# Kernel tuning notes

Hardware: AMD Instinct MI355X
Metric: run time of the kernel (lower is better)

The kernel has to match this reference:

```python
import jax, jax.numpy as jnp
import numpy as np

N_NODES = 10000
N_EDGES = 640000
D = 128


def _sage_conv(x, src, dst, W_l, b, W_r):
    # PyG SAGEConv (mean aggr): out = lin_l(mean_{j in N(i)} x_j) + lin_r(x_i)
    msgs = x[src]                                        # [E, D_in] gather
    agg = jax.ops.segment_sum(msgs, dst, num_segments=N_NODES)  # [N, D_in]
    deg = jax.ops.segment_sum(jnp.ones((src.shape[0],), x.dtype), dst,
                              num_segments=N_NODES)
    agg = agg / jnp.maximum(deg, 1.0)[:, None]           # mean; isolated nodes -> 0
    return agg @ W_l + b + x @ W_r


def setup_inputs() -> dict:
    key = jax.random.key(0)
    ks = jax.random.split(key, 8)
    s = 1.0 / np.sqrt(D)
    return {
        "x": jax.random.normal(ks[0], (N_NODES, D), dtype=jnp.float32),
        "edge_index": jax.random.randint(ks[1], (2, N_EDGES), 0, N_NODES, dtype=jnp.int64),
        "W_l0": jax.random.normal(ks[2], (D, D), dtype=jnp.float32) * s,
        "b0": jnp.zeros((D,), dtype=jnp.float32),
        "W_r0": jax.random.normal(ks[3], (D, D), dtype=jnp.float32) * s,
        "W_l1": jax.random.normal(ks[4], (D, D), dtype=jnp.float32) * s,
        "b1": jnp.zeros((D,), dtype=jnp.float32),
        "W_r1": jax.random.normal(ks[5], (D, D), dtype=jnp.float32) * s,
    }


def reference(x, edge_index, W_l0, b0, W_r0, W_l1, b1, W_r1):
    # Dropout(p=0.3) is identity in eval mode (reference runs inference math).
    src, dst = edge_index[0], edge_index[1]
    h = jax.nn.elu(_sage_conv(x, src, dst, W_l0, b0, W_r0))
    h = jax.nn.elu(_sage_conv(h, src, dst, W_l1, b1, W_r1))
    return h
```

## Files before the change

kernel.cpp:

```cpp
#include <hip/hip_runtime.h>

#define N_NODES 10000
#define N_EDGES 640000
#define D 128
#define MAXDEG 128
#define NBUCK 157
#define BCAP 6144
#define EPT 5
#define ZROW 10000

typedef unsigned int uint;
typedef unsigned short u16;
typedef short bf16x8 __attribute__((ext_vector_type(8)));
typedef float f32x4 __attribute__((ext_vector_type(4)));

__device__ __forceinline__ u16 f2bf(float f) {
    uint u = __float_as_uint(f);
    return (u16)((u + 0x7fffu + ((u >> 16) & 1u)) >> 16);
}
__device__ __forceinline__ float bflo(uint v) { return __uint_as_float(v << 16); }
__device__ __forceinline__ float bfhi(uint v) { return __uint_as_float(v & 0xffff0000u); }

__device__ __forceinline__ int edge_at(const void* ei, int is32, int idx) {
    if (is32) return ((const int*)ei)[idx];
    return (int)((const long long*)ei)[idx];
}

__global__ __launch_bounds__(256)
void binp1_kernel(const void* __restrict__ ei, int* __restrict__ gcount,
                  uint* __restrict__ gbucket) {
    __shared__ int hist[NBUCK];
    __shared__ int base[NBUCK];
    __shared__ int s_is32;
    const int t = threadIdx.x;
    if (t < NBUCK) hist[t] = 0;
    if (t == 0) s_is32 = 0;
    __syncthreads();
    const int e0 = blockIdx.x * (256 * EPT);
    if (((const int*)ei)[2 * (e0 + t) + 1] != 0) s_is32 = 1;
    __syncthreads();
    const int is32 = s_is32;
    uint pk[EPT];
    int  rk[EPT];
#pragma unroll
    for (int i = 0; i < EPT; ++i) {
        int e  = e0 + i * 256 + t;
        int s  = edge_at(ei, is32, e);
        int dn = edge_at(ei, is32, N_EDGES + e);
        pk[i] = ((uint)dn << 16) | (uint)s;
        rk[i] = atomicAdd(&hist[dn >> 6], 1);
    }
    __syncthreads();
    if (t < NBUCK) base[t] = atomicAdd(&gcount[t], hist[t]);
    __syncthreads();
#pragma unroll
    for (int i = 0; i < EPT; ++i) {
        int bkt = (int)(pk[i] >> 22);
        int pos = base[bkt] + rk[i];
        if (pos < BCAP) gbucket[(size_t)bkt * BCAP + pos] = pk[i];
    }
}

__global__ __launch_bounds__(256)
void prep_kernel(const int* __restrict__ gcount, const uint* __restrict__ gbucket,
                 u16* __restrict__ adj, int* __restrict__ deg_g,
                 const float* __restrict__ x, uint* __restrict__ xb2,
                 const float* __restrict__ Wl0, const float* __restrict__ Wr0,
                 const float* __restrict__ Wl1, const float* __restrict__ Wr1,
                 u16* __restrict__ WT0, u16* __restrict__ WT1) {
    const int b = blockIdx.x;
    const int t = threadIdx.x;
    __shared__ __align__(16) u16 tile[64][MAXDEG];
    __shared__ int cur[64];
    if (b < NBUCK) {
        uint* tw = (uint*)&tile[0][0];
#pragma unroll
        for (int q = 0; q < 16; ++q) tw[t + q * 256] = ((uint)ZROW << 16) | ZROW;
        if (t < 64) cur[t] = 0;
        __syncthreads();
        const int total = min(gcount[b], BCAP);
        for (int e = t; e < total; e += 256) {
            uint pk = gbucket[(size_t)b * BCAP + e];
            int ln = (int)((pk >> 16) & 63u);
            int r = atomicAdd(&cur[ln], 1);
            if (r < MAXDEG) tile[ln][r] = (u16)(pk & 0xffffu);
        }
        __syncthreads();
        const int node0 = b * 64;
        if (t < 64 && node0 + t < N_NODES) deg_g[node0 + t] = cur[t];
        const uint4* ts = (const uint4*)&tile[0][0];
#pragma unroll
        for (int q = 0; q < 4; ++q) {
            int i = t + q * 256;
            int node = node0 + (i >> 4);
            if (node < N_NODES) ((uint4*)(adj + (size_t)node * MAXDEG))[i & 15] = ts[i];
        }
    } else if (b < NBUCK + 625) {
        int idx = (b - NBUCK) * 256 + t;
        const float4* p = (const float4*)x + (size_t)idx * 2;
        float4 a = p[0], bb = p[1];
        uint4 r;
        r.x = (uint)f2bf(a.x) | ((uint)f2bf(a.y) << 16);
        r.y = (uint)f2bf(a.z) | ((uint)f2bf(a.w) << 16);
        r.z = (uint)f2bf(bb.x) | ((uint)f2bf(bb.y) << 16);
        r.w = (uint)f2bf(bb.z) | ((uint)f2bf(bb.w) << 16);
        ((uint4*)xb2)[idx] = r;
    } else if (b < NBUCK + 625 + 256) {
        int b2 = b - (NBUCK + 625);
        int layer = b2 >> 7, d = b2 & 127, k = t;
        const float* Wl = layer ? Wl1 : Wl0;
        const float* Wr = layer ? Wr1 : Wr0;
        u16* WT = layer ? WT1 : WT0;
        float v = (k < 128) ? Wl[k * D + d] : Wr[(k - 128) * D + d];
        WT[(size_t)d * 256 + k] = f2bf(v);
    } else {
        if (t < 16) ((uint4*)(xb2 + (size_t)ZROW * 64))[t] = make_uint4(0, 0, 0, 0);
    }
}

__global__ __launch_bounds__(256)
void gather_kernel(const uint* __restrict__ xb2, const u16* __restrict__ adj,
                   const int* __restrict__ deg_g, uint* __restrict__ aggb2) {
    const int node = blockIdx.x * 4 + (threadIdx.x >> 6);
    const int l = threadIdx.x & 63;
    const int g = l >> 4;
    const int c = l & 15;
    const int half = g >> 1;
    const int sh = (g & 1) << 4;
    const int dg = deg_g[node];
    const int cnt = min(dg, MAXDEG);
    const uint4* __restrict__ rowq = (const uint4*)(adj + (size_t)node * MAXDEG);
    float acc[8];
#pragma unroll
    for (int i = 0; i < 8; ++i) acc[i] = 0.f;
    const int nch = (cnt + 15) >> 4;
#pragma unroll 2
    for (int ch = 0; ch < nch; ++ch) {
        uint4 wa = rowq[2 * ch];
        uint4 wb = rowq[2 * ch + 1];
        uint a0 = half ? wa.y : wa.x;
        uint a1 = half ? wa.w : wa.z;
        uint b0 = half ? wb.y : wb.x;
        uint b1 = half ? wb.w : wb.z;
        uint id0 = (a0 >> sh) & 0xffffu;
        uint id1 = (a1 >> sh) & 0xffffu;
        uint id2 = (b0 >> sh) & 0xffffu;
        uint id3 = (b1 >> sh) & 0xffffu;
        uint4 v0 = ((const uint4*)(xb2 + (size_t)id0 * 64))[c];
        uint4 v1 = ((const uint4*)(xb2 + (size_t)id1 * 64))[c];
        uint4 v2 = ((const uint4*)(xb2 + (size_t)id2 * 64))[c];
        uint4 v3 = ((const uint4*)(xb2 + (size_t)id3 * 64))[c];
        acc[0] += bflo(v0.x) + bflo(v1.x) + bflo(v2.x) + bflo(v3.x);
        acc[1] += bfhi(v0.x) + bfhi(v1.x) + bfhi(v2.x) + bfhi(v3.x);
        acc[2] += bflo(v0.y) + bflo(v1.y) + bflo(v2.y) + bflo(v3.y);
        acc[3] += bfhi(v0.y) + bfhi(v1.y) + bfhi(v2.y) + bfhi(v3.y);
        acc[4] += bflo(v0.z) + bflo(v1.z) + bflo(v2.z) + bflo(v3.z);
        acc[5] += bfhi(v0.z) + bfhi(v1.z) + bfhi(v2.z) + bfhi(v3.z);
        acc[6] += bflo(v0.w) + bflo(v1.w) + bflo(v2.w) + bflo(v3.w);
        acc[7] += bfhi(v0.w) + bfhi(v1.w) + bfhi(v2.w) + bfhi(v3.w);
    }
#pragma unroll
    for (int i = 0; i < 8; ++i) {
        float r = acc[i];
        r += __shfl_xor(r, 16, 64);
        r += __shfl_xor(r, 32, 64);
        acc[i] = r;
    }
    if (g == 0) {
        float inv = 1.0f / fmaxf((float)dg, 1.0f);
        uint4 o;
        o.x = (uint)f2bf(acc[0] * inv) | ((uint)f2bf(acc[1] * inv) << 16);
        o.y = (uint)f2bf(acc[2] * inv) | ((uint)f2bf(acc[3] * inv) << 16);
        o.z = (uint)f2bf(acc[4] * inv) | ((uint)f2bf(acc[5] * inv) << 16);
        o.w = (uint)f2bf(acc[6] * inv) | ((uint)f2bf(acc[7] * inv) << 16);
        ((uint4*)(aggb2 + (size_t)node * 64))[c] = o;
    }
}

__global__ __launch_bounds__(256)
void mfma_gemm_kernel(const uint* __restrict__ aggb2, const uint* __restrict__ xb2,
                      const u16* __restrict__ WT, const float* __restrict__ bias,
                      float* __restrict__ outf ,
                      u16* __restrict__ outb ) {
    __shared__ __align__(16) u16 A_lds[16 * 256];
    const int t = threadIdx.x;
    const int nb = blockIdx.x * 16;
    {
        const int row = t >> 4, c = t & 15;
        const int node = nb + row;
        uint4 va = ((const uint4*)(aggb2 + (size_t)node * 64))[c];
        uint4 vx = ((const uint4*)(xb2  + (size_t)node * 64))[c];
        char* base = (char*)A_lds + row * 512;
        const int swz = (row & 7) << 4;
        *(uint4*)(base + ((c * 16) ^ swz))       = va;
        *(uint4*)(base + ((256 + c * 16) ^ swz)) = vx;
    }
    __syncthreads();

    const int w = t >> 6, l = t & 63;
    const int lr = l & 15, g = l >> 4;
    f32x4 acc0 = {0.f, 0.f, 0.f, 0.f}, acc1 = {0.f, 0.f, 0.f, 0.f};
    const char* abase = (const char*)A_lds + lr * 512;
    const int aswz = (lr & 7) << 4;
    const u16* wt0 = WT + (size_t)(w * 32 + lr) * 256;
    const u16* wt1 = WT + (size_t)(w * 32 + 16 + lr) * 256;
#pragma unroll
    for (int kk = 0; kk < 8; ++kk) {
        bf16x8 af  = *(const bf16x8*)(abase + ((kk * 64 + g * 16) ^ aswz));
        bf16x8 bf0 = *(const bf16x8*)(wt0 + kk * 32 + g * 8);
        bf16x8 bf1 = *(const bf16x8*)(wt1 + kk * 32 + g * 8);
        acc0 = __builtin_amdgcn_mfma_f32_16x16x32_bf16(af, bf0, acc0, 0, 0, 0);
        acc1 = __builtin_amdgcn_mfma_f32_16x16x32_bf16(af, bf1, acc1, 0, 0, 0);
    }

    const int col0 = w * 32 + lr, col1 = col0 + 16;
    const float b0v = bias[col0], b1v = bias[col1];
#pragma unroll
    for (int j = 0; j < 4; ++j) {
        const int node = nb + g * 4 + j;
        float v0 = acc0[j] + b0v; v0 = v0 > 0.f ? v0 : expm1f(v0);
        float v1 = acc1[j] + b1v; v1 = v1 > 0.f ? v1 : expm1f(v1);
        if (outf) {
            outf[(size_t)node * D + col0] = v0;
            outf[(size_t)node * D + col1] = v1;
        }
        if (outb) {
            outb[(size_t)node * D + col0] = f2bf(v0);
            outb[(size_t)node * D + col1] = f2bf(v1);
        }
    }
    if (outb && blockIdx.x == 0 && t < 16)
        ((uint4*)(outb + (size_t)ZROW * D))[t] = make_uint4(0, 0, 0, 0);
}

extern "C" void kernel_launch(void* const* d_in, const int* in_sizes, int n_in,
                              void* d_out, int out_size, void* d_ws, size_t ws_size,
                              hipStream_t stream) {
    const float* x   = (const float*)d_in[0];
    const void*  ei  = d_in[1];
    const float* Wl0 = (const float*)d_in[2];
    const float* b0  = (const float*)d_in[3];
    const float* Wr0 = (const float*)d_in[4];
    const float* Wl1 = (const float*)d_in[5];
    const float* b1  = (const float*)d_in[6];
    const float* Wr1 = (const float*)d_in[7];
    float* out = (float*)d_out;

    char* ws = (char*)d_ws;
    int*  gcount  = (int*)(ws + 1024);
    int*  deg     = (int*)(ws + 4096);
    u16*  adj     = (u16*)(ws + 65536);
    uint* gbucket = (uint*)(ws + 3145728);
    uint* yb2     = (uint*)(ws + 3145728);
    uint* aggb2   = (uint*)(ws + 5705984);
    uint* xb2     = (uint*)(ws + 8266240);
    u16*  WT0     = (u16*)(ws + 10826752);
    u16*  WT1     = (u16*)(ws + 10892288);

    hipMemsetAsync(ws, 0, 4096, stream);

    binp1_kernel<<<500, 256, 0, stream>>>(ei, gcount, gbucket);
    prep_kernel<<<NBUCK + 625 + 256 + 1, 256, 0, stream>>>(
        gcount, gbucket, adj, deg, x, xb2, Wl0, Wr0, Wl1, Wr1, WT0, WT1);

    gather_kernel<<<2500, 256, 0, stream>>>(xb2, adj, deg, aggb2);
    mfma_gemm_kernel<<<625, 256, 0, stream>>>(aggb2, xb2, WT0, b0, (float*)0, (u16*)yb2);

    gather_kernel<<<2500, 256, 0, stream>>>(yb2, adj, deg, aggb2);
    mfma_gemm_kernel<<<625, 256, 0, stream>>>(aggb2, yb2, WT1, b1, out, (u16*)0);
}
```

Baseline: 79.84 us.

## Fuse neighbor gather and MFMA linear layer into one kernel per layer

Merges the per-node mean-aggregation gather and the bf16 MFMA GEMM into a single kernel, so the aggregated row goes into LDS instead of a global aggb2 buffer. That removes two launches and the global write and read of the intermediate. Each block now handles only 4 nodes, so the 16-row MFMA tiles are three-quarters zero padding. The 128x256 weight matrix is also reloaded by every one of 2500 blocks rather than 625, which adds MFMA and weight-load cost. Workspace offsets are rearranged so the x and y buffers no longer overlap.

```diff
diff --git a/kernel.cpp b/kernel.cpp
--- a/kernel.cpp
+++ b/kernel.cpp
@@ -119,14 +119,19 @@
 }
 
 __global__ __launch_bounds__(256)
-void gather_kernel(const uint* __restrict__ xb2, const u16* __restrict__ adj,
-                   const int* __restrict__ deg_g, uint* __restrict__ aggb2) {
-    const int node = blockIdx.x * 4 + (threadIdx.x >> 6);
-    const int l = threadIdx.x & 63;
-    const int g = l >> 4;
-    const int c = l & 15;
-    const int half = g >> 1;
-    const int sh = (g & 1) << 4;
+void fused_layer_kernel(const uint* __restrict__ src2, const u16* __restrict__ adj,
+                        const int* __restrict__ deg_g, const u16* __restrict__ WT,
+                        const float* __restrict__ bias,
+                        float* __restrict__ outf ,
+                        u16* __restrict__ outb ) {
+    __shared__ __align__(16) u16 A_lds[4][256];
+    const int t = threadIdx.x;
+    const int w = t >> 6, l = t & 63;
+    const int nb = blockIdx.x * 4;
+    const int node = nb + w;
+
+    const int g = l >> 4, c = l & 15;
+    const int half = g >> 1, sh = (g & 1) << 4;
     const int dg = deg_g[node];
     const int cnt = min(dg, MAXDEG);
     const uint4* __restrict__ rowq = (const uint4*)(adj + (size_t)node * MAXDEG);
@@ -146,10 +151,10 @@
         uint id1 = (a1 >> sh) & 0xffffu;
         uint id2 = (b0 >> sh) & 0xffffu;
         uint id3 = (b1 >> sh) & 0xffffu;
-        uint4 v0 = ((const uint4*)(xb2 + (size_t)id0 * 64))[c];
-        uint4 v1 = ((const uint4*)(xb2 + (size_t)id1 * 64))[c];
-        uint4 v2 = ((const uint4*)(xb2 + (size_t)id2 * 64))[c];
-        uint4 v3 = ((const uint4*)(xb2 + (size_t)id3 * 64))[c];
+        uint4 v0 = ((const uint4*)(src2 + (size_t)id0 * 64))[c];
+        uint4 v1 = ((const uint4*)(src2 + (size_t)id1 * 64))[c];
+        uint4 v2 = ((const uint4*)(src2 + (size_t)id2 * 64))[c];
+        uint4 v3 = ((const uint4*)(src2 + (size_t)id3 * 64))[c];
         acc[0] += bflo(v0.x) + bflo(v1.x) + bflo(v2.x) + bflo(v3.x);
         acc[1] += bfhi(v0.x) + bfhi(v1.x) + bfhi(v2.x) + bfhi(v3.x);
         acc[2] += bflo(v0.y) + bflo(v1.y) + bflo(v2.y) + bflo(v3.y);
@@ -166,6 +171,8 @@
         r += __shfl_xor(r, 32, 64);
         acc[i] = r;
     }
+    char* arow = (char*)&A_lds[w][0];
+    const int swz = w << 4;
     if (g == 0) {
         float inv = 1.0f / fmaxf((float)dg, 1.0f);
         uint4 o;
@@ -173,60 +180,45 @@
         o.y = (uint)f2bf(acc[2] * inv) | ((uint)f2bf(acc[3] * inv) << 16);
         o.z = (uint)f2bf(acc[4] * inv) | ((uint)f2bf(acc[5] * inv) << 16);
         o.w = (uint)f2bf(acc[6] * inv) | ((uint)f2bf(acc[7] * inv) << 16);
-        ((uint4*)(aggb2 + (size_t)node * 64))[c] = o;
-    }
-}
-
-__global__ __launch_bounds__(256)
-void mfma_gemm_kernel(const uint* __restrict__ aggb2, const uint* __restrict__ xb2,
-                      const u16* __restrict__ WT, const float* __restrict__ bias,
-                      float* __restrict__ outf ,
-                      u16* __restrict__ outb ) {
-    __shared__ __align__(16) u16 A_lds[16 * 256];
-    const int t = threadIdx.x;
-    const int nb = blockIdx.x * 16;
-    {
-        const int row = t >> 4, c = t & 15;
-        const int node = nb + row;
-        uint4 va = ((const uint4*)(aggb2 + (size_t)node * 64))[c];
-        uint4 vx = ((const uint4*)(xb2  + (size_t)node * 64))[c];
-        char* base = (char*)A_lds + row * 512;
-        const int swz = (row & 7) << 4;
-        *(uint4*)(base + ((c * 16) ^ swz))       = va;
-        *(uint4*)(base + ((256 + c * 16) ^ swz)) = vx;
-    }
-    __syncthreads();
-
-    const int w = t >> 6, l = t & 63;
-    const int lr = l & 15, g = l >> 4;
+        *(uint4*)(arow + ((c * 16) ^ swz)) = o;
+    }
+    if (l < 16) {
+        uint4 vx = ((const uint4*)(src2 + (size_t)node * 64))[l];
+        *(uint4*)(arow + ((256 + l * 16) ^ swz)) = vx;
+    }
+    __syncthreads();
+
+    const int lr = l & 15, q = l >> 4;
     f32x4 acc0 = {0.f, 0.f, 0.f, 0.f}, acc1 = {0.f, 0.f, 0.f, 0.f};
-    const char* abase = (const char*)A_lds + lr * 512;
-    const int aswz = (lr & 7) << 4;
     const u16* wt0 = WT + (size_t)(w * 32 + lr) * 256;
     const u16* wt1 = WT + (size_t)(w * 32 + 16 + lr) * 256;
+    const char* abase = (const char*)&A_lds[lr & 3][0];
+    const int aswz = (lr & 3) << 4;
 #pragma unroll
     for (int kk = 0; kk < 8; ++kk) {
-        bf16x8 af  = *(const bf16x8*)(abase + ((kk * 64 + g * 16) ^ aswz));
-        bf16x8 bf0 = *(const bf16x8*)(wt0 + kk * 32 + g * 8);
-        bf16x8 bf1 = *(const bf16x8*)(wt1 + kk * 32 + g * 8);
+        bf16x8 af = {0, 0, 0, 0, 0, 0, 0, 0};
+        if (lr < 4) af = *(const bf16x8*)(abase + ((kk * 64 + q * 16) ^ aswz));
+        bf16x8 bf0 = *(const bf16x8*)(wt0 + kk * 32 + q * 8);
+        bf16x8 bf1 = *(const bf16x8*)(wt1 + kk * 32 + q * 8);
         acc0 = __builtin_amdgcn_mfma_f32_16x16x32_bf16(af, bf0, acc0, 0, 0, 0);
         acc1 = __builtin_amdgcn_mfma_f32_16x16x32_bf16(af, bf1, acc1, 0, 0, 0);
     }
-
-    const int col0 = w * 32 + lr, col1 = col0 + 16;
-    const float b0v = bias[col0], b1v = bias[col1];
-#pragma unroll
-    for (int j = 0; j < 4; ++j) {
-        const int node = nb + g * 4 + j;
-        float v0 = acc0[j] + b0v; v0 = v0 > 0.f ? v0 : expm1f(v0);
-        float v1 = acc1[j] + b1v; v1 = v1 > 0.f ? v1 : expm1f(v1);
-        if (outf) {
-            outf[(size_t)node * D + col0] = v0;
-            outf[(size_t)node * D + col1] = v1;
-        }
-        if (outb) {
-            outb[(size_t)node * D + col0] = f2bf(v0);
-            outb[(size_t)node * D + col1] = f2bf(v1);
+    if (q == 0) {
+        const int col0 = w * 32 + lr, col1 = col0 + 16;
+        const float b0v = bias[col0], b1v = bias[col1];
+#pragma unroll
+        for (int j = 0; j < 4; ++j) {
+            const int nd = nb + j;
+            float v0 = acc0[j] + b0v; v0 = v0 > 0.f ? v0 : expm1f(v0);
+            float v1 = acc1[j] + b1v; v1 = v1 > 0.f ? v1 : expm1f(v1);
+            if (outf) {
+                outf[(size_t)nd * D + col0] = v0;
+                outf[(size_t)nd * D + col1] = v1;
+            }
+            if (outb) {
+                outb[(size_t)nd * D + col0] = f2bf(v0);
+                outb[(size_t)nd * D + col1] = f2bf(v1);
+            }
         }
     }
     if (outb && blockIdx.x == 0 && t < 16)
@@ -251,11 +243,10 @@
     int*  deg     = (int*)(ws + 4096);
     u16*  adj     = (u16*)(ws + 65536);
     uint* gbucket = (uint*)(ws + 3145728);
-    uint* yb2     = (uint*)(ws + 3145728);
-    uint* aggb2   = (uint*)(ws + 5705984);
-    uint* xb2     = (uint*)(ws + 8266240);
-    u16*  WT0     = (u16*)(ws + 10826752);
-    u16*  WT1     = (u16*)(ws + 10892288);
+    uint* xb2     = (uint*)(ws + 7340032);
+    uint* yb2     = (uint*)(ws + 10485760);
+    u16*  WT0     = (u16*)(ws + 13631488);
+    u16*  WT1     = (u16*)(ws + 13697024);
 
     hipMemsetAsync(ws, 0, 4096, stream);
 
@@ -263,9 +254,8 @@
     prep_kernel<<<NBUCK + 625 + 256 + 1, 256, 0, stream>>>(
         gcount, gbucket, adj, deg, x, xb2, Wl0, Wr0, Wl1, Wr1, WT0, WT1);
 
-    gather_kernel<<<2500, 256, 0, stream>>>(xb2, adj, deg, aggb2);
-    mfma_gemm_kernel<<<625, 256, 0, stream>>>(aggb2, xb2, WT0, b0, (float*)0, (u16*)yb2);
-
-    gather_kernel<<<2500, 256, 0, stream>>>(yb2, adj, deg, aggb2);
-    mfma_gemm_kernel<<<625, 256, 0, stream>>>(aggb2, yb2, WT1, b1, out, (u16*)0);
-}
+    fused_layer_kernel<<<2500, 256, 0, stream>>>(xb2, adj, deg, WT0, b0,
+                                                 (float*)0, (u16*)yb2);
+    fused_layer_kernel<<<2500, 256, 0, stream>>>(yb2, adj, deg, WT1, b1,
+                                                 out, (u16*)0);
+}
```

Result: slower. 95.71 us (+19.9%).

## Replace global-atomic edge binning with per-chunk fixed segments and merge prep kernels

Applied to the files above, without the earlier changes.

Edge binning now writes each chunk's edges into a fixed per-(bucket, chunk) segment of 64 slots with a per-chunk count table, instead of reserving space through global atomics on bucket counters. That removes the hipMemsetAsync and folds the binning, x-to-bf16 conversion and weight transpose into a single launch, followed by a separate sort kernel that scans 500 chunk segments per bucket. The sort kernel now does many small, partly idle segment reads (each wave handles one chunk at a time), and edges beyond 64 per chunk-bucket pair would be dropped silently. For random edges that overflow is unlikely, but it is not guaranteed.

```diff
diff --git a/kernel.cpp b/kernel.cpp
--- a/kernel.cpp
+++ b/kernel.cpp
@@ -5,8 +5,9 @@
 #define D 128
 #define MAXDEG 128
 #define NBUCK 157
-#define BCAP 6144
-#define EPT 5
+#define NCHUNK 500
+#define CH_E 1280
+#define CSEG 64
 #define ZROW 10000
 
 typedef unsigned int uint;
@@ -27,76 +28,43 @@
 }
 
 __global__ __launch_bounds__(256)
-void binp1_kernel(const void* __restrict__ ei, int* __restrict__ gcount,
-                  uint* __restrict__ gbucket) {
-    __shared__ int hist[NBUCK];
-    __shared__ int base[NBUCK];
-    __shared__ int s_is32;
-    const int t = threadIdx.x;
-    if (t < NBUCK) hist[t] = 0;
-    if (t == 0) s_is32 = 0;
-    __syncthreads();
-    const int e0 = blockIdx.x * (256 * EPT);
-    if (((const int*)ei)[2 * (e0 + t) + 1] != 0) s_is32 = 1;
-    __syncthreads();
-    const int is32 = s_is32;
-    uint pk[EPT];
-    int  rk[EPT];
-#pragma unroll
-    for (int i = 0; i < EPT; ++i) {
-        int e  = e0 + i * 256 + t;
-        int s  = edge_at(ei, is32, e);
-        int dn = edge_at(ei, is32, N_EDGES + e);
-        pk[i] = ((uint)dn << 16) | (uint)s;
-        rk[i] = atomicAdd(&hist[dn >> 6], 1);
-    }
-    __syncthreads();
-    if (t < NBUCK) base[t] = atomicAdd(&gcount[t], hist[t]);
-    __syncthreads();
-#pragma unroll
-    for (int i = 0; i < EPT; ++i) {
-        int bkt = (int)(pk[i] >> 22);
-        int pos = base[bkt] + rk[i];
-        if (pos < BCAP) gbucket[(size_t)bkt * BCAP + pos] = pk[i];
-    }
-}
-
-__global__ __launch_bounds__(256)
-void prep_kernel(const int* __restrict__ gcount, const uint* __restrict__ gbucket,
-                 u16* __restrict__ adj, int* __restrict__ deg_g,
-                 const float* __restrict__ x, uint* __restrict__ xb2,
-                 const float* __restrict__ Wl0, const float* __restrict__ Wr0,
-                 const float* __restrict__ Wl1, const float* __restrict__ Wr1,
-                 u16* __restrict__ WT0, u16* __restrict__ WT1) {
+void binbig_kernel(const void* __restrict__ ei, u16* __restrict__ cnt,
+                   uint* __restrict__ gbucket2, const float* __restrict__ x,
+                   uint* __restrict__ xb2, uint* __restrict__ yb2,
+                   const float* __restrict__ Wl0, const float* __restrict__ Wr0,
+                   const float* __restrict__ Wl1, const float* __restrict__ Wr1,
+                   u16* __restrict__ WT0, u16* __restrict__ WT1) {
     const int b = blockIdx.x;
     const int t = threadIdx.x;
-    __shared__ __align__(16) u16 tile[64][MAXDEG];
-    __shared__ int cur[64];
-    if (b < NBUCK) {
-        uint* tw = (uint*)&tile[0][0];
-#pragma unroll
-        for (int q = 0; q < 16; ++q) tw[t + q * 256] = ((uint)ZROW << 16) | ZROW;
-        if (t < 64) cur[t] = 0;
+    if (b < NCHUNK) {
+        __shared__ int hist[NBUCK];
+        __shared__ int s_is32;
+        if (t < NBUCK) hist[t] = 0;
+        if (t == 0) s_is32 = 0;
         __syncthreads();
-        const int total = min(gcount[b], BCAP);
-        for (int e = t; e < total; e += 256) {
-            uint pk = gbucket[(size_t)b * BCAP + e];
-            int ln = (int)((pk >> 16) & 63u);
-            int r = atomicAdd(&cur[ln], 1);
-            if (r < MAXDEG) tile[ln][r] = (u16)(pk & 0xffffu);
-        }
+        if (((const int*)ei)[2 * t + 1] != 0) s_is32 = 1;
         __syncthreads();
-        const int node0 = b * 64;
-        if (t < 64 && node0 + t < N_NODES) deg_g[node0 + t] = cur[t];
-        const uint4* ts = (const uint4*)&tile[0][0];
-#pragma unroll
-        for (int q = 0; q < 4; ++q) {
-            int i = t + q * 256;
-            int node = node0 + (i >> 4);
-            if (node < N_NODES) ((uint4*)(adj + (size_t)node * MAXDEG))[i & 15] = ts[i];
-        }
-    } else if (b < NBUCK + 625) {
-        int idx = (b - NBUCK) * 256 + t;
+        const int is32 = s_is32;
+        const int e0 = b * CH_E;
+        uint pk[5]; int rk[5];
+#pragma unroll
+        for (int i = 0; i < 5; ++i) {
+            int e  = e0 + i * 256 + t;
+            int s  = edge_at(ei, is32, e);
+            int dn = edge_at(ei, is32, N_EDGES + e);
+            pk[i] = ((uint)dn << 16) | (uint)s;
+            rk[i] = atomicAdd(&hist[dn >> 6], 1);
+        }
+        __syncthreads();
+        if (t < NBUCK) cnt[(size_t)b * NBUCK + t] = (u16)min(hist[t], CSEG);
+#pragma unroll
+        for (int i = 0; i < 5; ++i) {
+            int bkt = (int)(pk[i] >> 22);
+            if (rk[i] < CSEG)
+                gbucket2[(size_t)bkt * (NCHUNK * CSEG) + b * CSEG + rk[i]] = pk[i];
+        }
+    } else if (b < NCHUNK + 625) {
+        int idx = (b - NCHUNK) * 256 + t;
         const float4* p = (const float4*)x + (size_t)idx * 2;
         float4 a = p[0], bb = p[1];
         uint4 r;
@@ -105,8 +73,8 @@
         r.z = (uint)f2bf(bb.x) | ((uint)f2bf(bb.y) << 16);
         r.w = (uint)f2bf(bb.z) | ((uint)f2bf(bb.w) << 16);
         ((uint4*)xb2)[idx] = r;
-    } else if (b < NBUCK + 625 + 256) {
-        int b2 = b - (NBUCK + 625);
+    } else if (b < NCHUNK + 625 + 256) {
+        int b2 = b - (NCHUNK + 625);
         int layer = b2 >> 7, d = b2 & 127, k = t;
         const float* Wl = layer ? Wl1 : Wl0;
         const float* Wr = layer ? Wr1 : Wr0;
@@ -114,7 +82,45 @@
         float v = (k < 128) ? Wl[k * D + d] : Wr[(k - 128) * D + d];
         WT[(size_t)d * 256 + k] = f2bf(v);
     } else {
-        if (t < 16) ((uint4*)(xb2 + (size_t)ZROW * 64))[t] = make_uint4(0, 0, 0, 0);
+        if (t < 16) {
+            ((uint4*)(xb2 + (size_t)ZROW * 64))[t] = make_uint4(0, 0, 0, 0);
+            ((uint4*)(yb2 + (size_t)ZROW * 64))[t] = make_uint4(0, 0, 0, 0);
+        }
+    }
+}
+
+__global__ __launch_bounds__(256)
+void sort_kernel(const u16* __restrict__ cnt, const uint* __restrict__ gbucket2,
+                 u16* __restrict__ adj, int* __restrict__ deg_g) {
+    __shared__ __align__(16) u16 tile[64][MAXDEG];
+    __shared__ int cur[64];
+    const int b = blockIdx.x;
+    const int t = threadIdx.x;
+    const int w = t >> 6, l = t & 63;
+    uint* tw = (uint*)&tile[0][0];
+#pragma unroll
+    for (int q = 0; q < 16; ++q) tw[t + q * 256] = ((uint)ZROW << 16) | ZROW;
+    if (t < 64) cur[t] = 0;
+    __syncthreads();
+    const uint* __restrict__ seg = gbucket2 + (size_t)b * (NCHUNK * CSEG);
+    for (int c = w; c < NCHUNK; c += 4) {
+        int n = cnt[(size_t)c * NBUCK + b];
+        if (l < n) {
+            uint pk = seg[c * CSEG + l];
+            int ln = (int)((pk >> 16) & 63u);
+            int r = atomicAdd(&cur[ln], 1);
+            if (r < MAXDEG) tile[ln][r] = (u16)(pk & 0xffffu);
+        }
+    }
+    __syncthreads();
+    const int node0 = b * 64;
+    if (t < 64 && node0 + t < N_NODES) deg_g[node0 + t] = cur[t];
+    const uint4* ts = (const uint4*)&tile[0][0];
+#pragma unroll
+    for (int q = 0; q < 4; ++q) {
+        int i = t + q * 256;
+        int node = node0 + (i >> 4);
+        if (node < N_NODES) ((uint4*)(adj + (size_t)node * MAXDEG))[i & 15] = ts[i];
     }
 }
 
@@ -128,12 +134,12 @@
     const int half = g >> 1;
     const int sh = (g & 1) << 4;
     const int dg = deg_g[node];
-    const int cnt = min(dg, MAXDEG);
+    const int cnt_ = min(dg, MAXDEG);
     const uint4* __restrict__ rowq = (const uint4*)(adj + (size_t)node * MAXDEG);
     float acc[8];
 #pragma unroll
     for (int i = 0; i < 8; ++i) acc[i] = 0.f;
-    const int nch = (cnt + 15) >> 4;
+    const int nch = (cnt_ + 15) >> 4;
 #pragma unroll 2
     for (int ch = 0; ch < nch; ++ch) {
         uint4 wa = rowq[2 * ch];
@@ -198,7 +204,7 @@
     __syncthreads();
 
     const int w = t >> 6, l = t & 63;
-    const int lr = l & 15, g = l >> 4;
+    const int lr = l & 15, q = l >> 4;
     f32x4 acc0 = {0.f, 0.f, 0.f, 0.f}, acc1 = {0.f, 0.f, 0.f, 0.f};
     const char* abase = (const char*)A_lds + lr * 512;
     const int aswz = (lr & 7) << 4;
@@ -206,9 +212,9 @@
     const u16* wt1 = WT + (size_t)(w * 32 + 16 + lr) * 256;
 #pragma unroll
     for (int kk = 0; kk < 8; ++kk) {
-        bf16x8 af  = *(const bf16x8*)(abase + ((kk * 64 + g * 16) ^ aswz));
-        bf16x8 bf0 = *(const bf16x8*)(wt0 + kk * 32 + g * 8);
-        bf16x8 bf1 = *(const bf16x8*)(wt1 + kk * 32 + g * 8);
+        bf16x8 af  = *(const bf16x8*)(abase + ((kk * 64 + q * 16) ^ aswz));
+        bf16x8 bf0 = *(const bf16x8*)(wt0 + kk * 32 + q * 8);
+        bf16x8 bf1 = *(const bf16x8*)(wt1 + kk * 32 + q * 8);
         acc0 = __builtin_amdgcn_mfma_f32_16x16x32_bf16(af, bf0, acc0, 0, 0, 0);
         acc1 = __builtin_amdgcn_mfma_f32_16x16x32_bf16(af, bf1, acc1, 0, 0, 0);
     }
@@ -217,7 +223,7 @@
     const float b0v = bias[col0], b1v = bias[col1];
 #pragma unroll
     for (int j = 0; j < 4; ++j) {
-        const int node = nb + g * 4 + j;
+        const int node = nb + q * 4 + j;
         float v0 = acc0[j] + b0v; v0 = v0 > 0.f ? v0 : expm1f(v0);
         float v1 = acc1[j] + b1v; v1 = v1 > 0.f ? v1 : expm1f(v1);
         if (outf) {
@@ -229,8 +235,6 @@
             outb[(size_t)node * D + col1] = f2bf(v1);
         }
     }
-    if (outb && blockIdx.x == 0 && t < 16)
-        ((uint4*)(outb + (size_t)ZROW * D))[t] = make_uint4(0, 0, 0, 0);
 }
 
 extern "C" void kernel_launch(void* const* d_in, const int* in_sizes, int n_in,
@@ -247,25 +251,24 @@
     float* out = (float*)d_out;
 
     char* ws = (char*)d_ws;
-    int*  gcount  = (int*)(ws + 1024);
-    int*  deg     = (int*)(ws + 4096);
-    u16*  adj     = (u16*)(ws + 65536);
-    uint* gbucket = (uint*)(ws + 3145728);
-    uint* yb2     = (uint*)(ws + 3145728);
-    uint* aggb2   = (uint*)(ws + 5705984);
-    uint* xb2     = (uint*)(ws + 8266240);
-    u16*  WT0     = (u16*)(ws + 10826752);
-    u16*  WT1     = (u16*)(ws + 10892288);
-
-    hipMemsetAsync(ws, 0, 4096, stream);
-
-    binp1_kernel<<<500, 256, 0, stream>>>(ei, gcount, gbucket);
-    prep_kernel<<<NBUCK + 625 + 256 + 1, 256, 0, stream>>>(
-        gcount, gbucket, adj, deg, x, xb2, Wl0, Wr0, Wl1, Wr1, WT0, WT1);
+    u16*  cnt      = (u16*)(ws + 1024);
+    int*  deg      = (int*)(ws + 262144);
+    u16*  adj      = (u16*)(ws + 1048576);
+    uint* gbucket2 = (uint*)(ws + 4194304);
+    uint* xb2      = (uint*)(ws + 25165824);
+    uint* yb2      = (uint*)(ws + 29360128);
+    uint* aggb2    = (uint*)(ws + 33554432);
+    u16*  WT0      = (u16*)(ws + 37748736);
+    u16*  WT1      = (u16*)(ws + 37879808);
+
+    binbig_kernel<<<NCHUNK + 625 + 256 + 1, 256, 0, stream>>>(
+        ei, cnt, gbucket2, x, xb2, yb2, Wl0, Wr0, Wl1, Wr1, WT0, WT1);
+    sort_kernel<<<NBUCK, 256, 0, stream>>>(cnt, gbucket2, adj, deg);
 
     gather_kernel<<<2500, 256, 0, stream>>>(xb2, adj, deg, aggb2);
-    mfma_gemm_kernel<<<625, 256, 0, stream>>>(aggb2, xb2, WT0, b0, (float*)0, (u16*)yb2);
-
+    mfma_gemm_kernel<<<625, 256, 0, stream>>>(aggb2, xb2, WT0, b0,
+                                              (float*)0, (u16*)yb2);
     gather_kernel<<<2500, 256, 0, stream>>>(yb2, adj, deg, aggb2);
-    mfma_gemm_kernel<<<625, 256, 0, stream>>>(aggb2, yb2, WT1, b1, out, (u16*)0);
-}
+    mfma_gemm_kernel<<<625, 256, 0, stream>>>(aggb2, yb2, WT1, b1,
+                                              out, (u16*)0);
+}
```

Measured after the change: 120.7 us. +51.1%, slower.
